# Optimization experiments

Measured on AMD Instinct MI355X. Metric: run time of the kernel, lower is better.

## Reference

```python
import jax, jax.numpy as jnp
import numpy as np

EMBED = 1024
HEAD_COUNT = 16
HEAD_DIM = EMBED // HEAD_COUNT  # 64


def setup_inputs() -> dict:
    key = jax.random.key(0)
    ks = jax.random.split(key, 5)
    N, S = 2, 1024
    keys_ = jax.random.normal(ks[0], (N, S, EMBED), dtype=jnp.float32)
    query = jax.random.normal(ks[1], (N, S, EMBED), dtype=jnp.float32)
    values = jax.random.normal(ks[2], (N, S, EMBED), dtype=jnp.float32)
    mask = jnp.ones((N, 1, S, S), dtype=jnp.int32)
    W_out = jax.random.normal(ks[3], (EMBED, EMBED), dtype=jnp.float32) * (1.0 / np.sqrt(EMBED))
    b_out = jax.random.normal(ks[4], (EMBED,), dtype=jnp.float32) * 0.01
    return {"keys": keys_, "query": query, "values": values, "mask": mask,
            "W_out": W_out, "b_out": b_out}


def reference(keys, query, values, mask, W_out, b_out):
    N, Sq, E = query.shape
    Sk = keys.shape[1]
    Sv = values.shape[1]
    # Faithful to the original: reshape to (N, L, head_dimensions, head_count);
    # einsum 'nqhd,nkhd->nhqk' uses h = head_dimensions (64) as the head axis.
    q = query.reshape(N, Sq, HEAD_DIM, HEAD_COUNT)
    k = keys.reshape(N, Sk, HEAD_DIM, HEAD_COUNT)
    v = values.reshape(N, Sv, HEAD_DIM, HEAD_COUNT)
    ene = jnp.einsum('nqhd,nkhd->nhqk', q, k)  # [N, 64, Sq, Sk]
    ene = jnp.where(mask == 0, jnp.float32(-1e20), ene)
    attn = jax.nn.softmax(ene / jnp.sqrt(jnp.float32(E)), axis=3)
    out = jnp.einsum('nhql,nlhd->nqhd', attn, v).reshape(N, Sq, EMBED)
    # forward_out Linear (with bias): y = x @ W.T + b
    return out @ W_out.T + b_out
```

## Files before the change

kernel.cpp:

```cpp
#include <hip/hip_runtime.h>
#include <hip/hip_bf16.h>


#define S_LEN 1024
#define EMB   1024
#define HD    16

typedef __attribute__((ext_vector_type(8)))  short short8;
typedef __attribute__((ext_vector_type(16))) float floatx16;

#if __has_builtin(__builtin_amdgcn_exp2f)
#define EXP2(x) __builtin_amdgcn_exp2f(x)
#else
#define EXP2(x) exp2f(x)
#endif

union PkU { __hip_bfloat162 h; unsigned int u; };
__device__ __forceinline__ unsigned int pk2(float a, float b) {
    PkU p; p.h = __float22bfloat162_rn(make_float2(a, b)); return p.u;
}
union Frag { unsigned int u[4]; short8 s; };

typedef const __attribute__((address_space(1))) unsigned int* gas1_t;
typedef __attribute__((address_space(3))) unsigned int* las3_t;
__device__ __forceinline__ void async_lds16(const void* g, void* lds) {
    __builtin_amdgcn_global_load_lds((gas1_t)g, (las3_t)lds, 16, 0, 0);
}

__global__ __launch_bounds__(256) void attn_kernel(
    const float* __restrict__ keys,
    const float* __restrict__ query,
    const float* __restrict__ values,
    unsigned short* __restrict__ xout)
{
    const int b   = blockIdx.x;
    const int hn  = b & 127;
    const int q0  = (b >> 7) * 128;
    const int h   = hn & 63;
    const int n   = hn >> 6;
    const int tid = threadIdx.x;
    const int w   = tid >> 6;
    const int l   = tid & 63;
    const int l31 = l & 31;
    const int hi  = l >> 5;

    __shared__ unsigned short VL[2][8 * 512];

    for (int i = tid; i < 2 * 8 * 512; i += 256)
        ((unsigned short*)VL)[i] =
            (((i >> 3) & 31) == 16) ? (unsigned short)0x3F80 : (unsigned short)0;

    const float* vptr[2]; int vdst[2];
    #pragma unroll
    for (int p = 0; p < 2; ++p) {
        int idx = tid + 256 * p;
        int vd  = idx & 15;
        int g4  = idx >> 4;
        int s   = g4 >> 2;
        int hi2 = (g4 >> 1) & 1;
        int jh  = g4 & 1;
        int key0 = s * 16 + 4 * hi2 + 8 * jh;
        vptr[p] = &values[(size_t)(n * S_LEN + key0) * EMB + h * HD + vd];
        vdst[p] = s * 512 + (vd + 32 * hi2) * 8 + 4 * jh;
    }

    const int q = q0 + 32 * w + l31;
    Frag qf;
    {
        const float* qp = &query[(size_t)(n * S_LEN + q) * EMB + h * HD + 8 * hi];
        float4 a  = *(const float4*)qp;
        float4 b4 = *(const float4*)(qp + 4);
        const float sc = 0.04508422009f;
        qf.u[0] = pk2(a.x * sc, a.y * sc);
        qf.u[1] = pk2(a.z * sc, a.w * sc);
        qf.u[2] = pk2(b4.x * sc, b4.y * sc);
        qf.u[3] = pk2(b4.z * sc, b4.w * sc);
    }

    const float* kbase = &keys[(size_t)(n * S_LEN + l31) * EMB + h * HD + 8 * hi];

    floatx16 O;
    #pragma unroll
    for (int i = 0; i < 16; ++i) O[i] = 0.0f;

    __syncthreads();

    float4 vpre[2];
    #pragma unroll
    for (int p = 0; p < 2; ++p) {
        const float* vp = vptr[p];
        vpre[p].x = vp[0];       vpre[p].y = vp[EMB];
        vpre[p].z = vp[2 * EMB]; vpre[p].w = vp[3 * EMB];
        vptr[p] += 128 * EMB;
    }
    #pragma unroll
    for (int p = 0; p < 2; ++p)
        *(uint2*)&VL[0][vdst[p]] =
            make_uint2(pk2(vpre[p].x, vpre[p].y), pk2(vpre[p].z, vpre[p].w));
    __syncthreads();

    for (int kt = 0; kt < 8; ++kt) {
        const int cur = kt & 1;
        const unsigned short* VLc = VL[cur];

        if (kt < 7) {
            #pragma unroll
            for (int p = 0; p < 2; ++p) {
                const float* vp = vptr[p];
                vpre[p].x = vp[0];       vpre[p].y = vp[EMB];
                vpre[p].z = vp[2 * EMB]; vpre[p].w = vp[3 * EMB];
                vptr[p] += 128 * EMB;
            }
        }

        #pragma unroll
        for (int t = 0; t < 4; ++t) {
            const float* kp = kbase + (size_t)(kt * 128 + t * 32) * EMB;
            float4 ka = *(const float4*)kp;
            float4 kb = *(const float4*)(kp + 4);
            Frag kf;
            kf.u[0] = pk2(ka.x, ka.y);
            kf.u[1] = pk2(ka.z, ka.w);
            kf.u[2] = pk2(kb.x, kb.y);
            kf.u[3] = pk2(kb.z, kb.w);

            floatx16 zc;
            #pragma unroll
            for (int i = 0; i < 16; ++i) zc[i] = 0.0f;
            floatx16 S = __builtin_amdgcn_mfma_f32_32x32x16_bf16(kf.s, qf.s, zc, 0, 0, 0);

            float pv[16];
            #pragma unroll
            for (int i = 0; i < 16; ++i) pv[i] = EXP2(S[i]);

            #pragma unroll
            for (int u = 0; u < 2; ++u) {
                Frag pf;
                pf.u[0] = pk2(pv[8 * u + 0], pv[8 * u + 1]);
                pf.u[1] = pk2(pv[8 * u + 2], pv[8 * u + 3]);
                pf.u[2] = pk2(pv[8 * u + 4], pv[8 * u + 5]);
                pf.u[3] = pk2(pv[8 * u + 6], pv[8 * u + 7]);

                Frag vf;
                vf.s = *(const short8*)&VLc[(2 * t + u) * 512 + l * 8];
                O = __builtin_amdgcn_mfma_f32_32x32x16_bf16(vf.s, pf.s, O, 0, 0, 0);
            }
        }

        if (kt < 7) {
            unsigned short* VLn = VL[cur ^ 1];
            #pragma unroll
            for (int p = 0; p < 2; ++p)
                *(uint2*)&VLn[vdst[p]] =
                    make_uint2(pk2(vpre[p].x, vpre[p].y), pk2(vpre[p].z, vpre[p].w));
        }
        __syncthreads();
    }

    float d  = O[8];
    float dd = __shfl_xor(d, 32, 64);
    float inv = 1.0f / (hi ? dd : d);

    unsigned short* op = &xout[(size_t)(n * S_LEN + q) * EMB + h * HD];
    int vb = 4 * hi;
    uint2 g0 = make_uint2(pk2(O[0] * inv, O[1] * inv), pk2(O[2] * inv, O[3] * inv));
    uint2 g1 = make_uint2(pk2(O[4] * inv, O[5] * inv), pk2(O[6] * inv, O[7] * inv));
    *(uint2*)(op + vb)     = g0;
    *(uint2*)(op + vb + 8) = g1;
}

__global__ __launch_bounds__(256) void cvtW_kernel(
    const float* __restrict__ W, unsigned short* __restrict__ Wb)
{
    int i = (blockIdx.x * 256 + threadIdx.x) * 4;
    float4 v = *(const float4*)&W[i];
    *(uint2*)&Wb[i] = make_uint2(pk2(v.x, v.y), pk2(v.z, v.w));
}

__global__ __launch_bounds__(256) void proj_kernel(
    const unsigned short* __restrict__ X,
    const unsigned short* __restrict__ Wb,
    const float* __restrict__ bias,
    float* __restrict__ Y)
{
    __shared__ unsigned short AL[2][16 * 512];
    __shared__ unsigned short BL[2][8 * 512];

    const int b   = blockIdx.x;
    const int nt2 = (b & 7) * 2 + (b >> 7);
    const int mt  = (b >> 3) & 15;
    const int m0  = mt * 128;
    const int n0  = nt2 * 64;
    const int tid = threadIdx.x;
    const int w   = tid >> 6;
    const int l   = tid & 63;
    const int l31 = l & 31;
    const int hi  = l >> 5;

    const unsigned short* gA[4];
    #pragma unroll
    for (int i = 0; i < 4; ++i)
        gA[i] = &X[(size_t)(m0 + 32 * w + l31) * 1024 + 8 * (2 * i + hi)];
    const unsigned short* gB[2];
    #pragma unroll
    for (int i = 0; i < 2; ++i) {
        int bb = 2 * w + i;
        gB[i] = &Wb[(size_t)(n0 + 32 * (bb >> 2) + l31) * 1024 + 8 * (2 * (bb & 3) + hi)];
    }

    floatx16 acc0, acc1;
    #pragma unroll
    for (int i = 0; i < 16; ++i) { acc0[i] = 0.0f; acc1[i] = 0.0f; }

    #pragma unroll
    for (int i = 0; i < 4; ++i) async_lds16(gA[i], &AL[0][(4 * w + i) * 512]);
    #pragma unroll
    for (int i = 0; i < 2; ++i) async_lds16(gB[i], &BL[0][(2 * w + i) * 512]);
    __syncthreads();

    for (int it = 0; it < 16; ++it) {
        const int cur = it & 1;
        if (it < 15) {
            const int k0n = (it + 1) * 64;
            #pragma unroll
            for (int i = 0; i < 4; ++i)
                async_lds16(gA[i] + k0n, &AL[cur ^ 1][(4 * w + i) * 512]);
            #pragma unroll
            for (int i = 0; i < 2; ++i)
                async_lds16(gB[i] + k0n, &BL[cur ^ 1][(2 * w + i) * 512]);
        }
        #pragma unroll
        for (int s = 0; s < 4; ++s) {
            Frag af, bf0, bf1;
            af.s  = *(const short8*)&AL[cur][(w * 4 + s) * 512 + l * 8];
            bf0.s = *(const short8*)&BL[cur][(0 * 4 + s) * 512 + l * 8];
            bf1.s = *(const short8*)&BL[cur][(1 * 4 + s) * 512 + l * 8];
            acc0 = __builtin_amdgcn_mfma_f32_32x32x16_bf16(af.s, bf0.s, acc0, 0, 0, 0);
            acc1 = __builtin_amdgcn_mfma_f32_32x32x16_bf16(af.s, bf1.s, acc1, 0, 0, 0);
        }
        __syncthreads();
    }

    #pragma unroll
    for (int u = 0; u < 2; ++u) {
        const floatx16& acc = u ? acc1 : acc0;
        const int e = n0 + 32 * u + l31;
        const float bv = bias[e];
        #pragma unroll
        for (int reg = 0; reg < 16; ++reg) {
            int m = m0 + 32 * w + (reg & 3) + 8 * (reg >> 2) + 4 * hi;
            Y[(size_t)m * 1024 + e] = acc[reg] + bv;
        }
    }
}

extern "C" void kernel_launch(void* const* d_in, const int* in_sizes, int n_in,
                              void* d_out, int out_size, void* d_ws, size_t ws_size,
                              hipStream_t stream) {
    const float* keys   = (const float*)d_in[0];
    const float* query  = (const float*)d_in[1];
    const float* values = (const float*)d_in[2];
    const float* W_out  = (const float*)d_in[4];
    const float* b_out  = (const float*)d_in[5];
    float* Y = (float*)d_out;

    unsigned short* xout = (unsigned short*)d_ws;
    unsigned short* Wb   = xout + (size_t)2048 * 1024;

    cvtW_kernel<<<1024, 256, 0, stream>>>(W_out, Wb);
    attn_kernel<<<1024, 256, 0, stream>>>(keys, query, values, xout);
    proj_kernel<<<256, 256, 0, stream>>>(xout, Wb, b_out, Y);
}
```

Measured before the change: 140.2 us.

## Split attention over key halves with combine pass and retile projection GEMM

Splits the attention kernel across two key halves (split-K flash-decoding style), doubling the grid to 2048 blocks. Each block writes unnormalized fp32 partial outputs and denominators. A new combine kernel sums the partials, normalizes and writes bf16, and also absorbs the weight conversion. The projection GEMM is retiled to 64x64 output tiles with a 128-wide K step and 512 blocks to raise occupancy. The cost is extra fp32 partial-result traffic (about 16MB of writes and reads) and one more launch-dependent pass.

```diff
diff --git a/kernel.cpp b/kernel.cpp
--- a/kernel.cpp
+++ b/kernel.cpp
@@ -31,18 +31,21 @@
     const float* __restrict__ keys,
     const float* __restrict__ query,
     const float* __restrict__ values,
-    unsigned short* __restrict__ xout)
+    float* __restrict__ Op,
+    float* __restrict__ Dp)
 {
-    const int b   = blockIdx.x;
-    const int hn  = b & 127;
-    const int q0  = (b >> 7) * 128;
-    const int h   = hn & 63;
-    const int n   = hn >> 6;
-    const int tid = threadIdx.x;
-    const int w   = tid >> 6;
-    const int l   = tid & 63;
-    const int l31 = l & 31;
-    const int hi  = l >> 5;
+    const int b    = blockIdx.x;
+    const int hn   = b & 127;
+    const int half = (b >> 7) & 1;
+    const int q0   = (b >> 8) * 128;
+    const int h    = hn & 63;
+    const int n    = hn >> 6;
+    const int kb0  = half * 512;
+    const int tid  = threadIdx.x;
+    const int w    = tid >> 6;
+    const int l    = tid & 63;
+    const int l31  = l & 31;
+    const int hi   = l >> 5;
 
     __shared__ unsigned short VL[2][8 * 512];
 
@@ -60,7 +63,7 @@
         int hi2 = (g4 >> 1) & 1;
         int jh  = g4 & 1;
         int key0 = s * 16 + 4 * hi2 + 8 * jh;
-        vptr[p] = &values[(size_t)(n * S_LEN + key0) * EMB + h * HD + vd];
+        vptr[p] = &values[(size_t)(n * S_LEN + kb0 + key0) * EMB + h * HD + vd];
         vdst[p] = s * 512 + (vd + 32 * hi2) * 8 + 4 * jh;
     }
 
@@ -77,7 +80,7 @@
         qf.u[3] = pk2(b4.z * sc, b4.w * sc);
     }
 
-    const float* kbase = &keys[(size_t)(n * S_LEN + l31) * EMB + h * HD + 8 * hi];
+    const float* kbase = &keys[(size_t)(n * S_LEN + kb0 + l31) * EMB + h * HD + 8 * hi];
 
     floatx16 O;
     #pragma unroll
@@ -99,11 +102,11 @@
             make_uint2(pk2(vpre[p].x, vpre[p].y), pk2(vpre[p].z, vpre[p].w));
     __syncthreads();
 
-    for (int kt = 0; kt < 8; ++kt) {
+    for (int kt = 0; kt < 4; ++kt) {
         const int cur = kt & 1;
         const unsigned short* VLc = VL[cur];
 
-        if (kt < 7) {
+        if (kt < 3) {
             #pragma unroll
             for (int p = 0; p < 2; ++p) {
                 const float* vp = vptr[p];
@@ -147,7 +150,7 @@
             }
         }
 
-        if (kt < 7) {
+        if (kt < 3) {
             unsigned short* VLn = VL[cur ^ 1];
             #pragma unroll
             for (int p = 0; p < 2; ++p)
@@ -157,24 +160,46 @@
         __syncthreads();
     }
 
-    float d  = O[8];
-    float dd = __shfl_xor(d, 32, 64);
-    float inv = 1.0f / (hi ? dd : d);
-
-    unsigned short* op = &xout[(size_t)(n * S_LEN + q) * EMB + h * HD];
+    float* op = &Op[(size_t)half * 2097152 + (size_t)(n * S_LEN + q) * EMB + h * HD];
     int vb = 4 * hi;
-    uint2 g0 = make_uint2(pk2(O[0] * inv, O[1] * inv), pk2(O[2] * inv, O[3] * inv));
-    uint2 g1 = make_uint2(pk2(O[4] * inv, O[5] * inv), pk2(O[6] * inv, O[7] * inv));
-    *(uint2*)(op + vb)     = g0;
-    *(uint2*)(op + vb + 8) = g1;
-}
-
-__global__ __launch_bounds__(256) void cvtW_kernel(
-    const float* __restrict__ W, unsigned short* __restrict__ Wb)
+    *(float4*)(op + vb)     = make_float4(O[0], O[1], O[2], O[3]);
+    *(float4*)(op + vb + 8) = make_float4(O[4], O[5], O[6], O[7]);
+
+    if (hi == 0)
+        Dp[(size_t)half * 131072 + (size_t)(n * 64 + h) * 1024 + q] = O[8];
+}
+
+__global__ __launch_bounds__(256) void combine_kernel(
+    const float* __restrict__ Op,
+    const float* __restrict__ Dp,
+    const float* __restrict__ W,
+    unsigned short* __restrict__ Wb,
+    unsigned short* __restrict__ xoutb)
 {
-    int i = (blockIdx.x * 256 + threadIdx.x) * 4;
-    float4 v = *(const float4*)&W[i];
-    *(uint2*)&Wb[i] = make_uint2(pk2(v.x, v.y), pk2(v.z, v.w));
+    const int bid = blockIdx.x;
+    const int tid = threadIdx.x;
+
+    if (bid < 1024) {
+        int i = bid * 1024 + tid * 4;
+        float4 v = *(const float4*)&W[i];
+        *(uint2*)&Wb[i] = make_uint2(pk2(v.x, v.y), pk2(v.z, v.w));
+    }
+
+    const int base = (bid * 256 + tid) * 4;
+    const int nn   = base >> 20;
+    const int rem  = base & 1048575;
+    const int q    = rem >> 10;
+    const int e    = rem & 1023;
+    const int h    = e >> 4;
+
+    float4 o1 = *(const float4*)&Op[base];
+    float4 o2 = *(const float4*)&Op[2097152 + base];
+    size_t di = (size_t)(nn * 64 + h) * 1024 + q;
+    float d = Dp[di] + Dp[131072 + di];
+    float inv = 1.0f / d;
+    *(uint2*)&xoutb[base] = make_uint2(
+        pk2((o1.x + o2.x) * inv, (o1.y + o2.y) * inv),
+        pk2((o1.z + o2.z) * inv, (o1.w + o2.w) * inv));
 }
 
 __global__ __launch_bounds__(256) void proj_kernel(
@@ -184,73 +209,71 @@
     float* __restrict__ Y)
 {
     __shared__ unsigned short AL[2][16 * 512];
-    __shared__ unsigned short BL[2][8 * 512];
+    __shared__ unsigned short BL[2][16 * 512];
 
     const int b   = blockIdx.x;
-    const int nt2 = (b & 7) * 2 + (b >> 7);
-    const int mt  = (b >> 3) & 15;
-    const int m0  = mt * 128;
-    const int n0  = nt2 * 64;
+    const int nt  = (b & 7) * 2 + ((b >> 3) & 1);
+    const int mt  = b >> 4;
+    const int m0  = mt * 64;
+    const int n0  = nt * 64;
     const int tid = threadIdx.x;
     const int w   = tid >> 6;
     const int l   = tid & 63;
     const int l31 = l & 31;
     const int hi  = l >> 5;
+    const int mh  = w & 1;
+    const int nh  = w >> 1;
 
     const unsigned short* gA[4];
-    #pragma unroll
-    for (int i = 0; i < 4; ++i)
-        gA[i] = &X[(size_t)(m0 + 32 * w + l31) * 1024 + 8 * (2 * i + hi)];
-    const unsigned short* gB[2];
-    #pragma unroll
-    for (int i = 0; i < 2; ++i) {
-        int bb = 2 * w + i;
-        gB[i] = &Wb[(size_t)(n0 + 32 * (bb >> 2) + l31) * 1024 + 8 * (2 * (bb & 3) + hi)];
-    }
-
-    floatx16 acc0, acc1;
-    #pragma unroll
-    for (int i = 0; i < 16; ++i) { acc0[i] = 0.0f; acc1[i] = 0.0f; }
-
-    #pragma unroll
-    for (int i = 0; i < 4; ++i) async_lds16(gA[i], &AL[0][(4 * w + i) * 512]);
-    #pragma unroll
-    for (int i = 0; i < 2; ++i) async_lds16(gB[i], &BL[0][(2 * w + i) * 512]);
+    const unsigned short* gB[4];
+    #pragma unroll
+    for (int i = 0; i < 4; ++i) {
+        int ab = 4 * w + i;
+        int ro = 32 * (ab >> 3) + l31;
+        int ko = 16 * (ab & 7) + 8 * hi;
+        gA[i] = &X [(size_t)(m0 + ro) * 1024 + ko];
+        gB[i] = &Wb[(size_t)(n0 + ro) * 1024 + ko];
+    }
+
+    floatx16 acc;
+    #pragma unroll
+    for (int i = 0; i < 16; ++i) acc[i] = 0.0f;
+
+    #pragma unroll
+    for (int i = 0; i < 4; ++i) {
+        int ab = 4 * w + i;
+        async_lds16(gA[i], &AL[0][ab * 512]);
+        async_lds16(gB[i], &BL[0][ab * 512]);
+    }
     __syncthreads();
 
-    for (int it = 0; it < 16; ++it) {
+    for (int it = 0; it < 8; ++it) {
         const int cur = it & 1;
-        if (it < 15) {
-            const int k0n = (it + 1) * 64;
-            #pragma unroll
-            for (int i = 0; i < 4; ++i)
-                async_lds16(gA[i] + k0n, &AL[cur ^ 1][(4 * w + i) * 512]);
-            #pragma unroll
-            for (int i = 0; i < 2; ++i)
-                async_lds16(gB[i] + k0n, &BL[cur ^ 1][(2 * w + i) * 512]);
+        if (it < 7) {
+            const int k0n = (it + 1) * 128;
+            #pragma unroll
+            for (int i = 0; i < 4; ++i) {
+                int ab = 4 * w + i;
+                async_lds16(gA[i] + k0n, &AL[cur ^ 1][ab * 512]);
+                async_lds16(gB[i] + k0n, &BL[cur ^ 1][ab * 512]);
+            }
         }
         #pragma unroll
-        for (int s = 0; s < 4; ++s) {
-            Frag af, bf0, bf1;
-            af.s  = *(const short8*)&AL[cur][(w * 4 + s) * 512 + l * 8];
-            bf0.s = *(const short8*)&BL[cur][(0 * 4 + s) * 512 + l * 8];
-            bf1.s = *(const short8*)&BL[cur][(1 * 4 + s) * 512 + l * 8];
-            acc0 = __builtin_amdgcn_mfma_f32_32x32x16_bf16(af.s, bf0.s, acc0, 0, 0, 0);
-            acc1 = __builtin_amdgcn_mfma_f32_32x32x16_bf16(af.s, bf1.s, acc1, 0, 0, 0);
+        for (int s = 0; s < 8; ++s) {
+            Frag af, bf;
+            af.s = *(const short8*)&AL[cur][(mh * 8 + s) * 512 + l * 8];
+            bf.s = *(const short8*)&BL[cur][(nh * 8 + s) * 512 + l * 8];
+            acc = __builtin_amdgcn_mfma_f32_32x32x16_bf16(af.s, bf.s, acc, 0, 0, 0);
         }
         __syncthreads();
     }
 
-    #pragma unroll
-    for (int u = 0; u < 2; ++u) {
-        const floatx16& acc = u ? acc1 : acc0;
-        const int e = n0 + 32 * u + l31;
-        const float bv = bias[e];
-        #pragma unroll
-        for (int reg = 0; reg < 16; ++reg) {
-            int m = m0 + 32 * w + (reg & 3) + 8 * (reg >> 2) + 4 * hi;
-            Y[(size_t)m * 1024 + e] = acc[reg] + bv;
-        }
+    const int e = n0 + 32 * nh + l31;
+    const float bv = bias[e];
+    #pragma unroll
+    for (int reg = 0; reg < 16; ++reg) {
+        int m = m0 + 32 * mh + (reg & 3) + 8 * (reg >> 2) + 4 * hi;
+        Y[(size_t)m * 1024 + e] = acc[reg] + bv;
     }
 }
 
@@ -264,10 +287,12 @@
     const float* b_out  = (const float*)d_in[5];
     float* Y = (float*)d_out;
 
-    unsigned short* xout = (unsigned short*)d_ws;
-    unsigned short* Wb   = xout + (size_t)2048 * 1024;
-
-    cvtW_kernel<<<1024, 256, 0, stream>>>(W_out, Wb);
-    attn_kernel<<<1024, 256, 0, stream>>>(keys, query, values, xout);
-    proj_kernel<<<256, 256, 0, stream>>>(xout, Wb, b_out, Y);
-}
+    float* Op = (float*)d_ws;
+    float* Dp = Op + (size_t)2 * 2097152;
+    unsigned short* Wb    = (unsigned short*)(Dp + (size_t)2 * 131072);
+    unsigned short* xoutb = Wb + (size_t)1024 * 1024;
+
+    attn_kernel<<<2048, 256, 0, stream>>>(keys, query, values, Op, Dp);
+    combine_kernel<<<2048, 256, 0, stream>>>(Op, Dp, W_out, Wb, xoutb);
+    proj_kernel<<<512, 256, 0, stream>>>(xoutb, Wb, b_out, Y);
+}
```

Result: slower. 151.1 us (+7.8%).
